# Kernel tuning notes

Measured on AMD Instinct MI355X. Metric: run time of the kernel, lower is better.

Reference implementation:

```python
import jax, jax.numpy as jnp
import numpy as np

B, T, D, H = 4, 1024, 1024, 16
HD = D // H  # 64
EPS = 1e-5


def _layernorm(x, g, b):
    mu = jnp.mean(x, axis=-1, keepdims=True)
    var = jnp.mean(jnp.square(x - mu), axis=-1, keepdims=True)
    return (x - mu) * jax.lax.rsqrt(var + EPS) * g + b


def _apply_rope(x, cos, sin):
    # x: (B, H, T, HD); cos/sin: (T, HD//2)
    d = x.shape[-1] // 2
    x1, x2 = x[..., :d], x[..., d:]
    cos = cos[None, None]
    sin = sin[None, None]
    return jnp.concatenate([x1 * cos - x2 * sin, x1 * sin + x2 * cos], axis=-1)


def setup_inputs() -> dict:
    key = jax.random.key(0)
    ks = jax.random.split(key, 8)
    s = 0.02
    x = jax.random.normal(ks[0], (B, T, D), jnp.float32)
    # RoPE tables
    pos = jnp.arange(T, dtype=jnp.float32)
    inv_freq = 1.0 / (10000.0 ** (jnp.arange(HD // 2, dtype=jnp.float32) / (HD // 2)))
    ang = pos[:, None] * inv_freq[None, :]  # (T, HD//2)
    rope_cos, rope_sin = jnp.cos(ang), jnp.sin(ang)
    # causal mask: True = masked out (module does ~attn_mask before SDPA)
    attn_mask = jnp.triu(jnp.ones((T, T), dtype=bool), k=1)
    params = dict(
        ln1_g=jnp.ones((D,), jnp.float32), ln1_b=jnp.zeros((D,), jnp.float32),
        w_qkv=jax.random.normal(ks[1], (D, 3 * D), jnp.float32) * s,
        b_qkv=jnp.zeros((3 * D,), jnp.float32),
        w_out=jax.random.normal(ks[2], (D, D), jnp.float32) * s,
        b_out=jnp.zeros((D,), jnp.float32),
        ln2_g=jnp.ones((D,), jnp.float32), ln2_b=jnp.zeros((D,), jnp.float32),
        w1=jax.random.normal(ks[3], (D, 4 * D), jnp.float32) * s,
        b1=jnp.zeros((4 * D,), jnp.float32),
        w2=jax.random.normal(ks[4], (4 * D, D), jnp.float32) * s,
        b2=jnp.zeros((D,), jnp.float32),
    )
    return dict(x=x, attn_mask=attn_mask, rope_cos=rope_cos, rope_sin=rope_sin, **params)


def reference(x, attn_mask, rope_cos, rope_sin, ln1_g, ln1_b, w_qkv, b_qkv,
              w_out, b_out, ln2_g, ln2_b, w1, b1, w2, b2):
    b, t, d = x.shape
    h = _layernorm(x, ln1_g, ln1_b)
    qkv = (h @ w_qkv + b_qkv).reshape(b, t, 3, H, HD)
    q, k, v = jnp.transpose(qkv, (2, 0, 3, 1, 4))  # each (B, H, T, HD)
    q = _apply_rope(q, rope_cos, rope_sin)
    k = _apply_rope(k, rope_cos, rope_sin)
    scale = 1.0 / jnp.sqrt(jnp.asarray(HD, x.dtype))
    scores = jnp.einsum('bhqd,bhkd->bhqk', q, k) * scale
    allowed = ~attn_mask  # True = attend
    neg = jnp.finfo(scores.dtype).min
    scores = jnp.where(allowed[None, None], scores, neg)
    probs = jax.nn.softmax(scores, axis=-1)
    attn = jnp.einsum('bhqk,bhkd->bhqd', probs, v)
    attn = jnp.transpose(attn, (0, 2, 1, 3)).reshape(b, t, d)
    x = x + (attn @ w_out + b_out)
    h2 = _layernorm(x, ln2_g, ln2_b)
    mlp = jax.nn.gelu(h2 @ w1 + b1, approximate=False) @ w2 + b2
    return x + mlp
```

## Files before the change

kernel.cpp:

```cpp
#include <hip/hip_runtime.h>
#include <hip/hip_bf16.h>
#include <cstdint>


typedef __bf16 bf16x8_t __attribute__((ext_vector_type(8)));
typedef float  f32x4_t  __attribute__((ext_vector_type(4)));

#define MFMA16(a, b, c) __builtin_amdgcn_mfma_f32_16x16x32_bf16((a), (b), (c), 0, 0, 0)

static constexpr int Bb = 4, T = 1024, D = 1024, NH = 16, HD = 64;
static constexpr int ROWS = Bb * T;
static constexpr int QKVN = 3 * D;

__device__ __forceinline__ float bf2f(__hip_bfloat16 v) { return __bfloat162float(v); }
__device__ __forceinline__ ushort f2bfbits(float v) {
    __hip_bfloat16 h = __float2bfloat16(v);
    return *reinterpret_cast<ushort*>(&h);
}
__device__ __forceinline__ float loadf(const void* p, size_t i, int isb16) {
    return isb16 ? bf2f(((const __hip_bfloat16*)p)[i]) : ((const float*)p)[i];
}
__device__ __forceinline__ int dtype16(const void* gref) {
    return (((const unsigned*)gref)[0] & 0xFFFFu) != 0u;
}
__device__ __forceinline__ void gld_lds16(const __hip_bfloat16* g, __hip_bfloat16* l) {
    __builtin_amdgcn_global_load_lds(
        (const __attribute__((address_space(1))) void*)g,
        (__attribute__((address_space(3))) void*)l, 16, 0, 0);
}

__device__ __forceinline__ void trans_tile(const void* B, __hip_bfloat16* BT,
                                           int K, int N, int k0, int n0, int isb16) {
    __shared__ ushort t[64][65];
#pragma unroll
    for (int it = 0; it < 16; ++it) {
        int idx = threadIdx.x + it * 256;
        int r = idx >> 6, c = idx & 63;
        t[c][r] = f2bfbits(loadf(B, (size_t)(k0 + r) * N + n0 + c, isb16));
    }
    __syncthreads();
#pragma unroll
    for (int it = 0; it < 16; ++it) {
        int idx = threadIdx.x + it * 256;
        int r = idx >> 6, c = idx & 63;
        reinterpret_cast<ushort*>(BT)[(size_t)(n0 + r) * K + k0 + c] = t[r][c];
    }
}

__global__ __launch_bounds__(256) void transpose_k(const void* __restrict__ B,
                                                   __hip_bfloat16* __restrict__ BT,
                                                   const void* __restrict__ gref,
                                                   int K, int N) {
    trans_tile(B, BT, K, N, blockIdx.y * 64, blockIdx.x * 64, dtype16(gref));
}

__global__ __launch_bounds__(256) void megatrans_k(const void* w_qkv, const void* w_out,
                                                   const void* w1, const void* w2,
                                                   __hip_bfloat16* wqkvT, __hip_bfloat16* woutT,
                                                   __hip_bfloat16* w1T, __hip_bfloat16* w2T,
                                                   const void* __restrict__ gref) {
    const int isb16 = dtype16(gref);
    int bid = blockIdx.x;
    const void* src; __hip_bfloat16* dst; int K, N, l;
    if (bid < 768)       { src = w_qkv; dst = wqkvT; K = 1024; N = 3072; l = bid; }
    else if (bid < 1024) { src = w_out; dst = woutT; K = 1024; N = 1024; l = bid - 768; }
    else if (bid < 2048) { src = w1;    dst = w1T;   K = 1024; N = 4096; l = bid - 1024; }
    else                 { src = w2;    dst = w2T;   K = 4096; N = 1024; l = bid - 2048; }
    const int nb = N / 64;
    trans_tile(src, dst, K, N, (l / nb) * 64, (l % nb) * 64, isb16);
}

__global__ __launch_bounds__(256) void ln_k(const void* __restrict__ x,
                                            const void* __restrict__ g,
                                            const void* __restrict__ bt,
                                            __hip_bfloat16* __restrict__ out,
                                            const void* __restrict__ gref) {
    const int isb16 = dtype16(gref);
    const int row = blockIdx.x, tid = threadIdx.x;
    const int lane = tid & 63, w = tid >> 6;

    float v[4];
    if (isb16) {
        ushort4 raw = reinterpret_cast<const ushort4*>((const __hip_bfloat16*)x + (size_t)row * D)[tid];
        v[0] = __uint_as_float(((unsigned)raw.x) << 16);
        v[1] = __uint_as_float(((unsigned)raw.y) << 16);
        v[2] = __uint_as_float(((unsigned)raw.z) << 16);
        v[3] = __uint_as_float(((unsigned)raw.w) << 16);
    } else {
        float4 f = reinterpret_cast<const float4*>((const float*)x + (size_t)row * D)[tid];
        v[0] = f.x; v[1] = f.y; v[2] = f.z; v[3] = f.w;
    }

    float s1 = v[0] + v[1] + v[2] + v[3];
    float s2 = v[0] * v[0] + v[1] * v[1] + v[2] * v[2] + v[3] * v[3];
#pragma unroll
    for (int off = 32; off >= 1; off >>= 1) {
        s1 += __shfl_xor(s1, off, 64);
        s2 += __shfl_xor(s2, off, 64);
    }
    __shared__ float r1[4], r2[4];
    if (lane == 0) { r1[w] = s1; r2[w] = s2; }
    __syncthreads();
    float t1 = r1[0] + r1[1] + r1[2] + r1[3];
    float t2 = r2[0] + r2[1] + r2[2] + r2[3];
    float mu  = t1 * (1.0f / D);
    float var = t2 * (1.0f / D) - mu * mu;
    float rstd = rsqrtf(var + 1e-5f);

    const int c = tid * 4;
#pragma unroll
    for (int j = 0; j < 4; j++) {
        float gv = loadf(g, c + j, isb16), bv = loadf(bt, c + j, isb16);
        out[(size_t)row * D + c + j] = __float2bfloat16((v[j] - mu) * rstd * gv + bv);
    }
}

template <int MODE, bool SPLIT>
__global__ __launch_bounds__(512, 2) void gemm256_k(const __hip_bfloat16* __restrict__ A,
                                                    const __hip_bfloat16* __restrict__ BT,
                                                    const void* __restrict__ bias,
                                                    void* __restrict__ C,
                                                    const void* __restrict__ gref,
                                                    int M, int N, int Kstride, int klen) {
    extern __shared__ __hip_bfloat16 LDSb[];

    const int tid  = threadIdx.x;
    const int lane = tid & 63, w = tid >> 6;
    const int quad = lane >> 4, l15 = lane & 15;
    const int n0 = blockIdx.x * 256, m0 = blockIdx.y * 256;
    const int wmL = (w >> 2) * 128;
    const int wnL = (w & 3) * 64;
    const int kbase = SPLIT ? blockIdx.z * klen : 0;
    const int NT = klen >> 5;

    const int L0 = w * 1024 + lane * 16;
    const int L1 = L0 + 8192;
    const int r0 = L0 >> 6,  k0e = ((L0 & 63) ^ (((L0 >> 9) & 1) << 5)) >> 1;
    const int r1 = L1 >> 6,  k1e = ((L1 & 63) ^ (((L1 >> 9) & 1) << 5)) >> 1;
    const __hip_bfloat16* AgS0 = A  + (size_t)(m0 + r0) * Kstride + kbase + k0e;
    const __hip_bfloat16* AgS1 = A  + (size_t)(m0 + r1) * Kstride + kbase + k1e;
    const __hip_bfloat16* BgS0 = BT + (size_t)(n0 + r0) * Kstride + kbase + k0e;
    const __hip_bfloat16* BgS1 = BT + (size_t)(n0 + r1) * Kstride + kbase + k1e;
    const int ldst0 = w * 512, ldst1 = w * 512 + 4096;

    const int kofs = (quad * 8) ^ ((l15 & 8) << 1);

    f32x4_t acc[8][4] = {};

#pragma unroll
    for (int t = 0; t < 3; ++t) {
        __hip_bfloat16* sA = LDSb + t * 8192;
        __hip_bfloat16* sB = LDSb + 32768 + t * 8192;
        const int ko = t * 32;
        gld_lds16(AgS0 + ko, sA + ldst0);
        gld_lds16(AgS1 + ko, sA + ldst1);
        gld_lds16(BgS0 + ko, sB + ldst0);
        gld_lds16(BgS1 + ko, sB + ldst1);
    }
    asm volatile("s_waitcnt vmcnt(8)" ::: "memory");
    __builtin_amdgcn_s_barrier();
    __builtin_amdgcn_sched_barrier(0);

    for (int t = 0; t < NT; ++t) {
        if (t) {
            if (t + 2 < NT)      { asm volatile("s_waitcnt vmcnt(8)" ::: "memory"); }
            else if (t + 1 < NT) { asm volatile("s_waitcnt vmcnt(4)" ::: "memory"); }
            else                 { asm volatile("s_waitcnt vmcnt(0)" ::: "memory"); }
            __builtin_amdgcn_s_barrier();
            __builtin_amdgcn_sched_barrier(0);
        }
        if (t + 3 < NT) {
            const int sl = (t + 3) & 3;
            __hip_bfloat16* sA = LDSb + sl * 8192;
            __hip_bfloat16* sB = LDSb + 32768 + sl * 8192;
            const int ko = (t + 3) * 32;
            gld_lds16(AgS0 + ko, sA + ldst0);
            gld_lds16(AgS1 + ko, sA + ldst1);
            gld_lds16(BgS0 + ko, sB + ldst0);
            gld_lds16(BgS1 + ko, sB + ldst1);
        }

        const __hip_bfloat16* sA = LDSb + (t & 3) * 8192;
        const __hip_bfloat16* sB = LDSb + 32768 + (t & 3) * 8192;
        bf16x8_t a[8], b[4];
#pragma unroll
        for (int mf = 0; mf < 8; ++mf)
            a[mf] = *reinterpret_cast<const bf16x8_t*>(&sA[(wmL + mf * 16 + l15) * 32 + kofs]);
#pragma unroll
        for (int nf = 0; nf < 4; ++nf)
            b[nf] = *reinterpret_cast<const bf16x8_t*>(&sB[(wnL + nf * 16 + l15) * 32 + kofs]);
        __builtin_amdgcn_s_setprio(1);
#pragma unroll
        for (int mf = 0; mf < 8; ++mf)
#pragma unroll
            for (int nf = 0; nf < 4; ++nf)
                acc[mf][nf] = MFMA16(a[mf], b[nf], acc[mf][nf]);
        __builtin_amdgcn_s_setprio(0);
    }

    __syncthreads();

    __hip_bfloat16* Cb;
    if constexpr (SPLIT) {
        const int z = blockIdx.z;
        if (z == 0)      Cb = (__hip_bfloat16*)C;
        else if (z == 1) Cb = (__hip_bfloat16*)C + (size_t)M * N;
        else if (z == 2) Cb = (__hip_bfloat16*)const_cast<void*>(bias);
        else             Cb = (__hip_bfloat16*)const_cast<void*>(gref);
    } else {
        Cb = (__hip_bfloat16*)C;
    }
    const int isb16 = (MODE == 3) ? 0 : dtype16(gref);
    __hip_bfloat16* E = LDSb;
#pragma unroll
    for (int nf = 0; nf < 4; ++nf) {
        const int cc = wnL + nf * 16 + l15;
        const float bsv = (MODE == 3) ? 0.0f : loadf(bias, n0 + cc, isb16);
#pragma unroll
        for (int mf = 0; mf < 8; ++mf) {
            const int rbase = wmL + mf * 16 + quad * 4;
#pragma unroll
            for (int r = 0; r < 4; ++r) {
                const int rr = rbase + r;
                float v = acc[mf][nf][r] + bsv;
                if constexpr (MODE == 2)
                    v = 0.5f * v * (1.0f + erff(v * 0.70710678118654752f));
                E[rr * 256 + ((cc + (((rr >> 2) & 15) << 4)) & 255)] = __float2bfloat16(v);
            }
        }
    }
    __syncthreads();
#pragma unroll
    for (int it = 0; it < 16; ++it) {
        const int r = it * 16 + (tid >> 5), c = (tid & 31) * 8;
        const int cs = (c + (((r >> 2) & 15) << 4)) & 255;
        uint4 d = *reinterpret_cast<const uint4*>(&E[r * 256 + cs]);
        *reinterpret_cast<uint4*>(&Cb[(size_t)(m0 + r) * N + n0 + c]) = d;
    }
}

template <int MODE, bool SPLIT>
__global__ __launch_bounds__(256) void gemm_k(const __hip_bfloat16* __restrict__ A,
                                              const __hip_bfloat16* __restrict__ BT,
                                              const void* __restrict__ bias,
                                              void* __restrict__ C,
                                              const void* __restrict__ gref,
                                              int M, int N, int Kstride, int klen) {
    __shared__ __hip_bfloat16 LB[16384];

    const int tid  = threadIdx.x;
    const int lane = tid & 63, w = tid >> 6;
    const int quad = lane >> 4, l15 = lane & 15;
    const int n0 = blockIdx.x * 128, m0 = blockIdx.y * 128;
    const int wm = (w >> 1) * 64, wn = (w & 1) * 64;
    const int kbase = SPLIT ? blockIdx.z * klen : 0;

    const int srow = lane >> 2, skk = (lane & 3) * 8;
    const __hip_bfloat16* Ag = A  + (size_t)(m0 + w * 16 + srow) * Kstride + kbase + skk;
    const __hip_bfloat16* Bg = BT + (size_t)(n0 + w * 16 + srow) * Kstride + kbase + skk;
    const int lwb = (w * 16) * 32;

    f32x4_t acc[4][4] = {};

    gld_lds16(Ag,                LB + lwb);
    gld_lds16(Ag + 64 * Kstride, LB + lwb + 64 * 32);
    gld_lds16(Bg,                LB + 8192 + lwb);
    gld_lds16(Bg + 64 * Kstride, LB + 8192 + lwb + 64 * 32);
    __syncthreads();

    int p = 0;
    for (int k0 = 0; k0 < klen; k0 += 32) {
        if (k0 + 32 < klen) {
            __hip_bfloat16* An = LB + (p ^ 1) * 4096;
            __hip_bfloat16* Bn = LB + 8192 + (p ^ 1) * 4096;
            gld_lds16(Ag + k0 + 32,                An + lwb);
            gld_lds16(Ag + k0 + 32 + 64 * Kstride, An + lwb + 64 * 32);
            gld_lds16(Bg + k0 + 32,                Bn + lwb);
            gld_lds16(Bg + k0 + 32 + 64 * Kstride, Bn + lwb + 64 * 32);
        }

        const __hip_bfloat16* Ac = LB + p * 4096;
        const __hip_bfloat16* Bc = LB + 8192 + p * 4096;
        bf16x8_t af[4], bfr[4];
#pragma unroll
        for (int t = 0; t < 4; t++) {
            af[t]  = *reinterpret_cast<const bf16x8_t*>(&Ac[(wm + t * 16 + l15) * 32 + quad * 8]);
            bfr[t] = *reinterpret_cast<const bf16x8_t*>(&Bc[(wn + t * 16 + l15) * 32 + quad * 8]);
        }
#pragma unroll
        for (int i = 0; i < 4; i++)
#pragma unroll
            for (int j = 0; j < 4; j++)
                acc[i][j] = MFMA16(af[i], bfr[j], acc[i][j]);

        __syncthreads();
        p ^= 1;
    }

    __hip_bfloat16* Cb;
    if constexpr (SPLIT) {
        const int z = blockIdx.z;
        if (z == 0)      Cb = (__hip_bfloat16*)C;
        else if (z == 1) Cb = (__hip_bfloat16*)C + (size_t)M * N;
        else if (z == 2) Cb = (__hip_bfloat16*)const_cast<void*>(bias);
        else             Cb = (__hip_bfloat16*)const_cast<void*>(gref);
    } else {
        Cb = (__hip_bfloat16*)C;
    }
    const int isb16 = (MODE == 3) ? 0 : dtype16(gref);
    __hip_bfloat16* E = LB;
#pragma unroll
    for (int j = 0; j < 4; j++) {
        const int cc = wn + j * 16 + l15;
        const float bsv = (MODE == 3) ? 0.0f : loadf(bias, n0 + cc, isb16);
#pragma unroll
        for (int i = 0; i < 4; i++) {
            const int rbase = wm + i * 16 + quad * 4;
#pragma unroll
            for (int r = 0; r < 4; r++) {
                const int rr = rbase + r;
                float v = acc[i][j][r] + bsv;
                if constexpr (MODE == 2)
                    v = 0.5f * v * (1.0f + erff(v * 0.70710678118654752f));
                E[rr * 128 + ((cc + (((rr >> 2) & 7) << 4)) & 127)] = __float2bfloat16(v);
            }
        }
    }
    __syncthreads();
#pragma unroll
    for (int it = 0; it < 8; it++) {
        const int r = it * 16 + (tid >> 4), c = (tid & 15) * 8;
        const int cs = (c + (((r >> 2) & 7) << 4)) & 127;
        uint4 d = *reinterpret_cast<const uint4*>(&E[r * 128 + cs]);
        *reinterpret_cast<uint4*>(&Cb[(size_t)(m0 + r) * N + n0 + c]) = d;
    }
}

__global__ __launch_bounds__(256) void reduce4_k(const __hip_bfloat16* __restrict__ p0,
                                                 const __hip_bfloat16* __restrict__ p1,
                                                 const __hip_bfloat16* __restrict__ p2,
                                                 const __hip_bfloat16* __restrict__ p3,
                                                 const void* __restrict__ bias,
                                                 const void* __restrict__ res,
                                                 void* __restrict__ out,
                                                 const void* __restrict__ gref) {
    const int isb16 = dtype16(gref);
    const size_t i = ((size_t)blockIdx.x * 256 + threadIdx.x) * 4;
    ushort4 a = *reinterpret_cast<const ushort4*>(p0 + i);
    ushort4 b = *reinterpret_cast<const ushort4*>(p1 + i);
    ushort4 c = *reinterpret_cast<const ushort4*>(p2 + i);
    ushort4 d = *reinterpret_cast<const ushort4*>(p3 + i);
    const int col = (int)(i & (D - 1));
    float v[4];
    v[0] = __uint_as_float((unsigned)a.x << 16) + __uint_as_float((unsigned)b.x << 16)
         + __uint_as_float((unsigned)c.x << 16) + __uint_as_float((unsigned)d.x << 16);
    v[1] = __uint_as_float((unsigned)a.y << 16) + __uint_as_float((unsigned)b.y << 16)
         + __uint_as_float((unsigned)c.y << 16) + __uint_as_float((unsigned)d.y << 16);
    v[2] = __uint_as_float((unsigned)a.z << 16) + __uint_as_float((unsigned)b.z << 16)
         + __uint_as_float((unsigned)c.z << 16) + __uint_as_float((unsigned)d.z << 16);
    v[3] = __uint_as_float((unsigned)a.w << 16) + __uint_as_float((unsigned)b.w << 16)
         + __uint_as_float((unsigned)c.w << 16) + __uint_as_float((unsigned)d.w << 16);
#pragma unroll
    for (int j = 0; j < 4; j++)
        v[j] += loadf(bias, col + j, isb16) + loadf(res, i + j, isb16);
    if (isb16) {
        ushort4 o;
        o.x = f2bfbits(v[0]); o.y = f2bfbits(v[1]); o.z = f2bfbits(v[2]); o.w = f2bfbits(v[3]);
        *reinterpret_cast<ushort4*>((__hip_bfloat16*)out + i) = o;
    } else {
        float4 o = {v[0], v[1], v[2], v[3]};
        *reinterpret_cast<float4*>((float*)out + i) = o;
    }
}

__global__ __launch_bounds__(256) void gemm64_k(const __hip_bfloat16* __restrict__ A,
                                                const __hip_bfloat16* __restrict__ BT,
                                                const void* __restrict__ bias,
                                                const void* __restrict__ res,
                                                void* __restrict__ C,
                                                const void* __restrict__ gref,
                                                int M, int N, int K, int crow0) {
    __shared__ __hip_bfloat16 LB64[12288];

    const int tid  = threadIdx.x;
    const int lane = tid & 63, w = tid >> 6;
    const int quad = lane >> 4, l15 = lane & 15;
    const int n0 = blockIdx.x * 64, m0 = blockIdx.y * 128;
    const int wm = (w >> 1) * 64, wn = (w & 1) * 32;

    const int srow = lane >> 2, skk = (lane & 3) * 8;
    const __hip_bfloat16* Ag = A  + (size_t)(m0 + w * 16 + srow) * K + skk;
    const __hip_bfloat16* Bg = BT + (size_t)(n0 + w * 16 + srow) * K + skk;
    const int lwb = (w * 16) * 32;

    f32x4_t acc[4][2] = {};

    gld_lds16(Ag,          LB64 + lwb);
    gld_lds16(Ag + 64 * K, LB64 + lwb + 64 * 32);
    gld_lds16(Bg,          LB64 + 8192 + lwb);
    __syncthreads();

    int p = 0;
    for (int k0 = 0; k0 < K; k0 += 32) {
        if (k0 + 32 < K) {
            __hip_bfloat16* An = LB64 + (p ^ 1) * 4096;
            __hip_bfloat16* Bn = LB64 + 8192 + (p ^ 1) * 2048;
            gld_lds16(Ag + k0 + 32,          An + lwb);
            gld_lds16(Ag + k0 + 32 + 64 * K, An + lwb + 64 * 32);
            gld_lds16(Bg + k0 + 32,          Bn + lwb);
        }

        const __hip_bfloat16* Ac = LB64 + p * 4096;
        const __hip_bfloat16* Bc = LB64 + 8192 + p * 2048;
        bf16x8_t af[4], bfr[2];
#pragma unroll
        for (int t = 0; t < 4; t++)
            af[t]  = *reinterpret_cast<const bf16x8_t*>(&Ac[(wm + t * 16 + l15) * 32 + quad * 8]);
#pragma unroll
        for (int t = 0; t < 2; t++)
            bfr[t] = *reinterpret_cast<const bf16x8_t*>(&Bc[(wn + t * 16 + l15) * 32 + quad * 8]);
#pragma unroll
        for (int i = 0; i < 4; i++)
#pragma unroll
            for (int j = 0; j < 2; j++)
                acc[i][j] = MFMA16(af[i], bfr[j], acc[i][j]);

        __syncthreads();
        p ^= 1;
    }

    const int isb16 = dtype16(gref);
#pragma unroll
    for (int j = 0; j < 2; j++) {
        const int col = n0 + wn + j * 16 + l15;
        const float bsv = loadf(bias, col, isb16);
#pragma unroll
        for (int i = 0; i < 4; i++) {
            const int rbase = m0 + wm + i * 16 + quad * 4;
#pragma unroll
            for (int r = 0; r < 4; r++) {
                const size_t gr = (size_t)(crow0 + rbase + r);
                float v = acc[i][j][r] + bsv + loadf(res, gr * N + col, isb16);
                if (isb16) ((__hip_bfloat16*)C)[gr * N + col] = __float2bfloat16(v);
                else       ((float*)C)[gr * N + col] = v;
            }
        }
    }
}

__global__ __launch_bounds__(256) void ropevt_k(__hip_bfloat16* __restrict__ qkv,
                                                const void* __restrict__ rc,
                                                const void* __restrict__ rs,
                                                __hip_bfloat16* __restrict__ vT,
                                                const void* __restrict__ gref) {
    const int bid = blockIdx.x;
    if (bid < 8192) {
        const int isb16 = dtype16(gref);
        const int id = bid * 256 + threadIdx.x;
        const int d  = id & 31;
        const int h  = (id >> 5) & 15;
        const int t  = (id >> 9) & 1023;
        const int b  = id >> 19;
        const float c = loadf(rc, t * 32 + d, isb16);
        const float s = loadf(rs, t * 32 + d, isb16);
        __hip_bfloat16* base = qkv + ((size_t)(b * T + t)) * QKVN + h * HD + d;
        float x1 = bf2f(base[0]), x2 = bf2f(base[32]);
        base[0]  = __float2bfloat16((x1 * c - x2 * s) * 0.125f);
        base[32] = __float2bfloat16((x1 * s + x2 * c) * 0.125f);
        float y1 = bf2f(base[D]), y2 = bf2f(base[D + 32]);
        base[D]      = __float2bfloat16(y1 * c - y2 * s);
        base[D + 32] = __float2bfloat16(y1 * s + y2 * c);
    } else {
        __shared__ ushort t[64][65];
        const int l = bid - 8192;
        const int t0 = (l & 15) * 64, bh = l >> 4;
        const int b = bh >> 4, h = bh & 15;
        const __hip_bfloat16* src = qkv + ((size_t)b * T) * QKVN + 2 * D + h * HD;
#pragma unroll
        for (int it = 0; it < 16; ++it) {
            int idx = threadIdx.x + it * 256;
            int r = idx >> 6, d = idx & 63;
            t[d][r] = *reinterpret_cast<const ushort*>(src + (size_t)(t0 + r) * QKVN + d);
        }
        __syncthreads();
#pragma unroll
        for (int it = 0; it < 16; ++it) {
            int idx = threadIdx.x + it * 256;
            int r = idx >> 6, c = idx & 63;
            reinterpret_cast<ushort*>(vT)[((size_t)bh * 64 + r) * T + t0 + c] = t[r][c];
        }
    }
}

__global__ __launch_bounds__(256) void flash_k(const __hip_bfloat16* __restrict__ qkv,
                                               const __hip_bfloat16* __restrict__ vT,
                                               __hip_bfloat16* __restrict__ out) {
    __shared__ __hip_bfloat16 Qs[2][64 * 32];
    __shared__ __hip_bfloat16 Ks[2][2][64 * 32];
    __shared__ __hip_bfloat16 Vs[2][2][64 * 32];
    __shared__ __hip_bfloat16 Ps[4][2][16 * 32];

    const int tid = threadIdx.x;
    const int bid = blockIdx.x;
    const int qt = 15 - (bid >> 6);
    const int bh = bid & 63;
    const int b = bh >> 4, h = bh & 15;
    const int q0 = qt * 64;
    const int lane = tid & 63, w = tid >> 6, quad = lane >> 4, l15 = lane & 15;
    const int srow = lane >> 2, skk = (lane & 3) * 8;

    const __hip_bfloat16* qg = qkv + ((size_t)(b * T) + q0 + w * 16 + srow) * QKVN + h * HD + skk;
    const __hip_bfloat16* kg = qkv + ((size_t)(b * T) + w * 16 + srow) * QKVN + D + h * HD + skk;
    const __hip_bfloat16* vg = vT + ((size_t)bh * 64 + w * 16 + srow) * T + skk;

    gld_lds16(qg,      &Qs[0][(w * 16) * 32]);
    gld_lds16(qg + 32, &Qs[1][(w * 16) * 32]);
    gld_lds16(kg,      &Ks[0][0][(w * 16) * 32]);
    gld_lds16(kg + 32, &Ks[0][1][(w * 16) * 32]);
    gld_lds16(vg,      &Vs[0][0][(w * 16) * 32]);
    gld_lds16(vg + 32, &Vs[0][1][(w * 16) * 32]);
    __syncthreads();

    const bf16x8_t aq0 = *reinterpret_cast<const bf16x8_t*>(&Qs[0][(w * 16 + l15) * 32 + quad * 8]);
    const bf16x8_t aq1 = *reinterpret_cast<const bf16x8_t*>(&Qs[1][(w * 16 + l15) * 32 + quad * 8]);

    float m_run[4], l_run[4];
    f32x4_t o[4] = {};
#pragma unroll
    for (int i = 0; i < 4; i++) { m_run[i] = -1e30f; l_run[i] = 0.0f; }

    int p = 0;
    for (int kt = 0; kt <= qt; kt++) {
        if (kt < qt) {
            const size_t ko = (size_t)(kt + 1) * 64;
            gld_lds16(kg + ko * QKVN,      &Ks[p ^ 1][0][(w * 16) * 32]);
            gld_lds16(kg + ko * QKVN + 32, &Ks[p ^ 1][1][(w * 16) * 32]);
            gld_lds16(vg + ko,             &Vs[p ^ 1][0][(w * 16) * 32]);
            gld_lds16(vg + ko + 32,        &Vs[p ^ 1][1][(w * 16) * 32]);
        }

        f32x4_t s[4];
#pragma unroll
        for (int c = 0; c < 4; c++) {
            f32x4_t z = {};
            bf16x8_t k0f = *reinterpret_cast<const bf16x8_t*>(&Ks[p][0][(c * 16 + l15) * 32 + quad * 8]);
            bf16x8_t k1f = *reinterpret_cast<const bf16x8_t*>(&Ks[p][1][(c * 16 + l15) * 32 + quad * 8]);
            z = MFMA16(aq0, k0f, z);
            z = MFMA16(aq1, k1f, z);
            s[c] = z;
        }

        if (kt == qt) {
#pragma unroll
            for (int c = 0; c < 4; c++)
#pragma unroll
                for (int i = 0; i < 4; i++) {
                    int rr = w * 16 + quad * 4 + i;
                    int cc = c * 16 + l15;
                    if (cc > rr) s[c][i] = -1e30f;
                }
        }

        float mnew[4], alpha[4];
#pragma unroll
        for (int i = 0; i < 4; i++) {
            float mx = fmaxf(fmaxf(s[0][i], s[1][i]), fmaxf(s[2][i], s[3][i]));
#pragma unroll
            for (int off = 1; off < 16; off <<= 1) mx = fmaxf(mx, __shfl_xor(mx, off, 64));
            mnew[i] = fmaxf(m_run[i], mx);
            alpha[i] = __expf(m_run[i] - mnew[i]);
            m_run[i] = mnew[i];
        }
#pragma unroll
        for (int c = 0; c < 4; c++)
#pragma unroll
            for (int i = 0; i < 4; i++) s[c][i] = __expf(s[c][i] - mnew[i]);
#pragma unroll
        for (int i = 0; i < 4; i++) {
            float sm = s[0][i] + s[1][i] + s[2][i] + s[3][i];
#pragma unroll
            for (int off = 1; off < 16; off <<= 1) sm += __shfl_xor(sm, off, 64);
            l_run[i] = l_run[i] * alpha[i] + sm;
#pragma unroll
            for (int od = 0; od < 4; od++) o[od][i] *= alpha[i];
        }

#pragma unroll
        for (int c = 0; c < 4; c++)
#pragma unroll
            for (int i = 0; i < 4; i++)
                Ps[w][c >> 1][(quad * 4 + i) * 32 + (c & 1) * 16 + l15] =
                    __float2bfloat16(s[c][i]);

        bf16x8_t ap0 = *reinterpret_cast<const bf16x8_t*>(&Ps[w][0][l15 * 32 + quad * 8]);
        bf16x8_t ap1 = *reinterpret_cast<const bf16x8_t*>(&Ps[w][1][l15 * 32 + quad * 8]);
#pragma unroll
        for (int od = 0; od < 4; od++) {
            bf16x8_t v0f = *reinterpret_cast<const bf16x8_t*>(&Vs[p][0][(od * 16 + l15) * 32 + quad * 8]);
            bf16x8_t v1f = *reinterpret_cast<const bf16x8_t*>(&Vs[p][1][(od * 16 + l15) * 32 + quad * 8]);
            o[od] = MFMA16(ap0, v0f, o[od]);
            o[od] = MFMA16(ap1, v1f, o[od]);
        }

        __syncthreads();
        p ^= 1;
    }

#pragma unroll
    for (int od = 0; od < 4; od++)
#pragma unroll
        for (int i = 0; i < 4; i++) {
            int row = q0 + w * 16 + quad * 4 + i;
            int col = h * HD + od * 16 + l15;
            float v = o[od][i] / l_run[i];
            out[((size_t)b * T + row) * D + col] = __float2bfloat16(v);
        }
}

extern "C" void kernel_launch(void* const* d_in, const int* in_sizes, int n_in,
                              void* d_out, int out_size, void* d_ws, size_t ws_size,
                              hipStream_t stream) {
    const int o = (in_sizes[1] == T * (HD / 2)) ? 1 : 2;
    const void* x     = d_in[0];
    const void* rc    = d_in[o + 0];
    const void* rs    = d_in[o + 1];
    const void* ln1g  = d_in[o + 2];
    const void* ln1b  = d_in[o + 3];
    const void* w_qkv = d_in[o + 4];
    const void* b_qkv = d_in[o + 5];
    const void* w_out = d_in[o + 6];
    const void* b_out = d_in[o + 7];
    const void* ln2g  = d_in[o + 8];
    const void* ln2b  = d_in[o + 9];
    const void* w1    = d_in[o + 10];
    const void* b1    = d_in[o + 11];
    const void* w2    = d_in[o + 12];
    const void* b2    = d_in[o + 13];

    char* ws = (char*)d_ws;
    const size_t MB = 1024 * 1024;

    static bool attr_done = false;
    if (!attr_done) {
        hipFuncSetAttribute(reinterpret_cast<const void*>(&gemm256_k<0, false>),
                            hipFuncAttributeMaxDynamicSharedMemorySize, 131072);
        hipFuncSetAttribute(reinterpret_cast<const void*>(&gemm256_k<2, false>),
                            hipFuncAttributeMaxDynamicSharedMemorySize, 131072);
        hipFuncSetAttribute(reinterpret_cast<const void*>(&gemm256_k<3, true>),
                            hipFuncAttributeMaxDynamicSharedMemorySize, 131072);
        attr_done = true;
    }

    if (ws_size >= 72 * MB + 256) {
        __hip_bfloat16* bufA  = (__hip_bfloat16*)(ws + 256);
        __hip_bfloat16* qkvb  = (__hip_bfloat16*)(ws + 8 * MB + 256);
        __hip_bfloat16* vTb   = (__hip_bfloat16*)(ws + 32 * MB + 256);
        __hip_bfloat16* mid   = qkvb;
        __hip_bfloat16* wqkvT = (__hip_bfloat16*)(ws + 40 * MB + 256);
        __hip_bfloat16* woutT = (__hip_bfloat16*)(ws + 46 * MB + 256);
        __hip_bfloat16* w1T   = (__hip_bfloat16*)(ws + 48 * MB + 256);
        __hip_bfloat16* w2T   = (__hip_bfloat16*)(ws + 56 * MB + 256);
        __hip_bfloat16* part0 = (__hip_bfloat16*)(ws + 40 * MB + 256);
        __hip_bfloat16* part2 = (__hip_bfloat16*)(ws + 64 * MB + 256);
        __hip_bfloat16* part1 = (__hip_bfloat16*)(ws + 48 * MB + 256);
        __hip_bfloat16* part3 = bufA;

        megatrans_k<<<3072, 256, 0, stream>>>(w_qkv, w_out, w1, w2,
                                              wqkvT, woutT, w1T, w2T, ln1g);
        ln_k<<<ROWS, 256, 0, stream>>>(x, ln1g, ln1b, bufA, ln1g);
        gemm256_k<0, false><<<dim3(QKVN / 256, ROWS / 256), 512, 131072, stream>>>(
            bufA, wqkvT, b_qkv, qkvb, ln1g, ROWS, QKVN, D, D);
        ropevt_k<<<8192 + 1024, 256, 0, stream>>>(qkvb, rc, rs, vTb, ln1g);
        flash_k<<<16 * Bb * NH, 256, 0, stream>>>(qkvb, vTb, bufA);
        gemm64_k<<<dim3(D / 64, ROWS / 128), 256, 0, stream>>>(bufA, woutT, b_out, x,
                                                               d_out, ln1g, ROWS, D, D, 0);
        ln_k<<<ROWS, 256, 0, stream>>>(d_out, ln2g, ln2b, bufA, ln1g);
        gemm256_k<2, false><<<dim3(4 * D / 256, ROWS / 256), 512, 131072, stream>>>(
            bufA, w1T, b1, mid, ln1g, ROWS, 4 * D, D, D);
        gemm256_k<3, true><<<dim3(D / 256, ROWS / 256, 4), 512, 131072, stream>>>(
            mid, w2T, part2, part0, part3, ROWS, D, 4 * D, D);
        reduce4_k<<<(ROWS * D) / (256 * 4), 256, 0, stream>>>(part0, part1, part2, part3,
                                                              b2, d_out, d_out, ln1g);
    } else {
        __hip_bfloat16* bufA  = (__hip_bfloat16*)(ws + 256);
        __hip_bfloat16* qkvb  = (__hip_bfloat16*)(ws + 8 * MB + 256);
        __hip_bfloat16* wqkvT = (__hip_bfloat16*)(ws + 32 * MB + 256);
        __hip_bfloat16* vTb   = (__hip_bfloat16*)(ws + 32 * MB + 256);
        __hip_bfloat16* woutT = (__hip_bfloat16*)(ws + 8 * MB + 256);
        __hip_bfloat16* w1T   = (__hip_bfloat16*)(ws + 8 * MB + 256);
        __hip_bfloat16* w2T   = (__hip_bfloat16*)(ws + 16 * MB + 256);
        __hip_bfloat16* mid   = (__hip_bfloat16*)(ws + 24 * MB + 256);

        transpose_k<<<dim3(QKVN / 64, D / 64), 256, 0, stream>>>(w_qkv, wqkvT, ln1g, D, QKVN);
        ln_k<<<ROWS, 256, 0, stream>>>(x, ln1g, ln1b, bufA, ln1g);
        gemm_k<0, false><<<dim3(QKVN / 128, ROWS / 128), 256, 0, stream>>>(
            bufA, wqkvT, b_qkv, qkvb, ln1g, ROWS, QKVN, D, D);
        ropevt_k<<<8192 + 1024, 256, 0, stream>>>(qkvb, rc, rs, vTb, ln1g);
        flash_k<<<16 * Bb * NH, 256, 0, stream>>>(qkvb, vTb, bufA);
        transpose_k<<<dim3(D / 64, D / 64), 256, 0, stream>>>(w_out, woutT, ln1g, D, D);
        gemm64_k<<<dim3(D / 64, ROWS / 128), 256, 0, stream>>>(bufA, woutT, b_out, x,
                                                               d_out, ln1g, ROWS, D, D, 0);
        ln_k<<<ROWS, 256, 0, stream>>>(d_out, ln2g, ln2b, bufA, ln1g);
        transpose_k<<<dim3(4 * D / 64, D / 64), 256, 0, stream>>>(w1, w1T, ln1g, D, 4 * D);
        transpose_k<<<dim3(D / 64, 4 * D / 64), 256, 0, stream>>>(w2, w2T, ln1g, 4 * D, D);
        for (int c = 0; c < 2; c++) {
            const int ro = c * 2048;
            gemm_k<2, false><<<dim3(4 * D / 128, 2048 / 128), 256, 0, stream>>>(
                bufA + (size_t)ro * D, w1T, b1, mid, ln1g, 2048, 4 * D, D, D);
            gemm64_k<<<dim3(D / 64, 2048 / 128), 256, 0, stream>>>(mid, w2T, b2, d_out,
                                                                   d_out, ln1g, 2048, D, 4 * D, ro);
        }
    }
}
```

Measured before the change: 372.8 us.

## Split GEMM k-step into two halves interleaving LDS reads, prefetch and MFMA

Restructures the GEMM main loop so each k-step runs in two phases. Each phase loads half the A fragments from LDS, issues half the global-to-LDS prefetch (A, then B), waits on lgkmcnt, then runs 16 MFMAs, with extra barriers between phases. The aim is to interleave memory issue with matrix work and lower register pressure from held A fragments. The cost is two extra workgroup barriers per iteration, which could stall waves.

```diff
diff --git a/kernel.cpp b/kernel.cpp
--- a/kernel.cpp
+++ b/kernel.cpp
@@ -169,33 +169,59 @@
             __builtin_amdgcn_s_barrier();
             __builtin_amdgcn_sched_barrier(0);
         }
-        if (t + 3 < NT) {
-            const int sl = (t + 3) & 3;
-            __hip_bfloat16* sA = LDSb + sl * 8192;
-            __hip_bfloat16* sB = LDSb + 32768 + sl * 8192;
-            const int ko = (t + 3) * 32;
-            gld_lds16(AgS0 + ko, sA + ldst0);
-            gld_lds16(AgS1 + ko, sA + ldst1);
-            gld_lds16(BgS0 + ko, sB + ldst0);
-            gld_lds16(BgS1 + ko, sB + ldst1);
-        }
 
         const __hip_bfloat16* sA = LDSb + (t & 3) * 8192;
         const __hip_bfloat16* sB = LDSb + 32768 + (t & 3) * 8192;
-        bf16x8_t a[8], b[4];
-#pragma unroll
-        for (int mf = 0; mf < 8; ++mf)
+        const bool pf = (t + 3 < NT);
+        const int sl = (t + 3) & 3;
+        __hip_bfloat16* nA = LDSb + sl * 8192;
+        __hip_bfloat16* nB = LDSb + 32768 + sl * 8192;
+        const int ko = (t + 3) * 32;
+
+        bf16x8_t a[4], b[4];
+#pragma unroll
+        for (int mf = 0; mf < 4; ++mf)
             a[mf] = *reinterpret_cast<const bf16x8_t*>(&sA[(wmL + mf * 16 + l15) * 32 + kofs]);
 #pragma unroll
         for (int nf = 0; nf < 4; ++nf)
             b[nf] = *reinterpret_cast<const bf16x8_t*>(&sB[(wnL + nf * 16 + l15) * 32 + kofs]);
+        if (pf) {
+            gld_lds16(AgS0 + ko, nA + ldst0);
+            gld_lds16(AgS1 + ko, nA + ldst1);
+        }
+        __builtin_amdgcn_sched_barrier(0);
+        __builtin_amdgcn_s_barrier();
+        asm volatile("s_waitcnt lgkmcnt(0)" ::: "memory");
+        __builtin_amdgcn_sched_barrier(0);
         __builtin_amdgcn_s_setprio(1);
 #pragma unroll
-        for (int mf = 0; mf < 8; ++mf)
+        for (int mf = 0; mf < 4; ++mf)
 #pragma unroll
             for (int nf = 0; nf < 4; ++nf)
                 acc[mf][nf] = MFMA16(a[mf], b[nf], acc[mf][nf]);
         __builtin_amdgcn_s_setprio(0);
+        __builtin_amdgcn_sched_barrier(0);
+        __builtin_amdgcn_s_barrier();
+
+        bf16x8_t a2[4];
+#pragma unroll
+        for (int mf = 0; mf < 4; ++mf)
+            a2[mf] = *reinterpret_cast<const bf16x8_t*>(&sA[(wmL + 64 + mf * 16 + l15) * 32 + kofs]);
+        if (pf) {
+            gld_lds16(BgS0 + ko, nB + ldst0);
+            gld_lds16(BgS1 + ko, nB + ldst1);
+        }
+        __builtin_amdgcn_sched_barrier(0);
+        asm volatile("s_waitcnt lgkmcnt(0)" ::: "memory");
+        __builtin_amdgcn_sched_barrier(0);
+        __builtin_amdgcn_s_setprio(1);
+#pragma unroll
+        for (int mf = 0; mf < 4; ++mf)
+#pragma unroll
+            for (int nf = 0; nf < 4; ++nf)
+                acc[4 + mf][nf] = MFMA16(a2[mf], b[nf], acc[4 + mf][nf]);
+        __builtin_amdgcn_s_setprio(0);
+        __builtin_amdgcn_sched_barrier(0);
     }
 
     __syncthreads();
```

New measurement: 374.5 us. About the same (+0.5%).
